# Optimization experiments

Hardware: AMD Instinct MI355X
Metric: run time of the kernel (lower is better)

## Reference

```python
import jax, jax.numpy as jnp
import numpy as np

E, I, D = 8, 2816, 1024   # num_experts, intermediate_size, dim
T, A = 1024, 2            # tokens, top-k experts per token


def setup_inputs() -> dict:
    key = jax.random.key(0)
    k1, k2, k3, k4, k5 = jax.random.split(key, 5)
    x = jax.random.normal(k1, (T, D), dtype=jnp.float32)
    expert_indices = jax.random.randint(k2, (T, A), 0, E, dtype=jnp.int64)
    scale = 0.02
    w1 = jax.random.normal(k3, (E, I, D), dtype=jnp.float32) * scale
    w2 = jax.random.normal(k4, (E, D, I), dtype=jnp.float32) * scale
    w3 = jax.random.normal(k5, (E, I, D), dtype=jnp.float32) * scale
    return {"x": x, "w1": w1, "w2": w2, "w3": w3, "expert_indices": expert_indices}


def reference(x, w1, w2, w3, expert_indices):
    # x: [T, D], expert_indices: [T, A]
    # Same math as torch: silu(x @ w1[e].T) * (x @ w3[e].T) @ w2[e].T per (t, a).
    # Compute all-expert projections once, then gather the selected expert rows
    # (avoids materializing the [T, A, I, D] per-token weight copies).
    idx = expert_indices.astype(jnp.int32)
    h1 = jnp.einsum('ti,eoi->teo', x, w1)              # [T, E, I]
    h3 = jnp.einsum('ti,eoi->teo', x, w3)              # [T, E, I]
    g1 = jnp.take_along_axis(h1, idx[:, :, None], axis=1)  # [T, A, I]
    g3 = jnp.take_along_axis(h3, idx[:, :, None], axis=1)  # [T, A, I]
    h = jax.nn.silu(g1) * g3                            # SwiGLU, [T, A, I]
    y_all = jnp.einsum('tao,eio->taei', h, w2)          # [T, A, E, D]
    out = jnp.take_along_axis(y_all, idx[:, :, None, None], axis=2)  # [T, A, 1, D]
    return out[:, :, 0, :]                              # [T, A, D]
```

## Files before the change

### kernel.cpp

```cpp
#include <hip/hip_runtime.h>
#include <hip/hip_bf16.h>

#define E_NUM 8
#define I_DIM 2816
#define D_DIM 1024
#define T_NUM 1024
#define A_TOP 2
#define NPAIR (T_NUM * A_TOP)
#define PADROWS 3072
#define MT_MAX (PADROWS / 128)

#define HB_OFF    16384ULL
#define HB_BYTES  ((unsigned long long)PADROWS * I_DIM * 2ULL)
#define XBF_OFF   (HB_OFF + HB_BYTES)
#define XBF_BYTES ((unsigned long long)T_NUM * D_DIM * 2ULL)
#define WS_NEED   (XBF_OFF + XBF_BYTES)

typedef __bf16 bf16x8 __attribute__((ext_vector_type(8)));
typedef float  f32x4  __attribute__((ext_vector_type(4)));

__device__ inline unsigned short f2bf(float f) {
  union { float f; unsigned u; } v; v.f = f;
  unsigned r = v.u + 0x7fffu + ((v.u >> 16) & 1u);
  return (unsigned short)(r >> 16);
}
__device__ inline uint4 pack8(float4 a, float4 b) {
  uint4 v;
  v.x = (unsigned)f2bf(a.x) | ((unsigned)f2bf(a.y) << 16);
  v.y = (unsigned)f2bf(a.z) | ((unsigned)f2bf(a.w) << 16);
  v.z = (unsigned)f2bf(b.x) | ((unsigned)f2bf(b.y) << 16);
  v.w = (unsigned)f2bf(b.z) | ((unsigned)f2bf(b.w) << 16);
  return v;
}
__device__ inline void gload_lds16(const unsigned short* g, unsigned short* l) {
  __builtin_amdgcn_global_load_lds((const __attribute__((address_space(1))) void*)g,
                                   (__attribute__((address_space(3))) void*)l, 16, 0, 0);
}

__global__ __launch_bounds__(256) void sort_pairs_kernel(
    const int* __restrict__ eidx, int* __restrict__ meta, int* __restrict__ pairs)
{
  __shared__ int cnt[E_NUM];
  __shared__ int pstart[E_NUM + 1];
  __shared__ int cur[E_NUM];
  int tid = threadIdx.x;
  if (tid < E_NUM) cnt[tid] = 0;
  __syncthreads();
  for (int p = tid; p < NPAIR; p += 256) atomicAdd(&cnt[eidx[p] & 7], 1);
  for (int i = tid; i < PADROWS; i += 256) pairs[i] = -1;
  __syncthreads();
  if (tid == 0) {
    int s = 0;
    for (int e = 0; e < E_NUM; ++e) {
      pstart[e] = s; cur[e] = s;
      s += ((cnt[e] + 127) / 128) * 128;
    }
    pstart[E_NUM] = s;
  }
  __syncthreads();
  for (int p = tid; p < NPAIR; p += 256) {
    int e = eidx[p] & 7;
    int pos = atomicAdd(&cur[e], 1);
    pairs[pos] = p;
  }
  __syncthreads();
  if (tid <= E_NUM) meta[tid] = pstart[tid];
}

__global__ __launch_bounds__(256) void convertx_kernel(
    const float* __restrict__ in, unsigned short* __restrict__ out)
{
  size_t i = (size_t)(blockIdx.x * 256 + threadIdx.x) * 8;
  const float4* p = (const float4*)(in + i);
  *(uint4*)(out + i) = pack8(p[0], p[1]);
}

__global__ __launch_bounds__(256, 2) void stage1_fused(
    const unsigned short* __restrict__ xbf, const float* __restrict__ w1,
    const float* __restrict__ w3, const int* __restrict__ meta,
    const int* __restrict__ pairs, unsigned short* __restrict__ hbuf)
{
  int mtile = blockIdx.y;
  int ptotal = meta[E_NUM];
  if (mtile * 128 >= ptotal) return;
  int e = 0;
  while (meta[e + 1] <= mtile * 128) ++e;
  int ntile = blockIdx.x;

  __shared__ alignas(16) unsigned short As[2][128 * 32];
  __shared__ alignas(16) unsigned short B1s[2][128 * 32];
  __shared__ alignas(16) unsigned short B3s[2][128 * 32];
  __shared__ int rowtok[128];

  int tid = threadIdx.x;
  for (int i = tid; i < 128; i += 256) {
    int p = pairs[mtile * 128 + i];
    rowtok[i] = (p >= 0) ? (p >> 1) : -1;
  }
  __syncthreads();

  int lane = tid & 63;
  int w = tid >> 6;
  int wm = w >> 1, wn = w & 1;
  int lrow = lane & 15, quad = lane >> 4;

  int lr4 = lane >> 2;
  int lc  = (lane & 3) * 8;
  int c0 = 2 * w;
  size_t aoff[2];
  const float* wb1[2];
  const float* wb3[2];
#pragma unroll
  for (int j = 0; j < 2; ++j) {
    int c = c0 + j;
    int r = c * 16 + lr4;
    int tok = rowtok[r]; if (tok < 0) tok = 0;
    aoff[j] = (size_t)tok * D_DIM + lc;
    int irow = ntile * 128 + r;
    wb1[j] = w1 + ((size_t)e * I_DIM + irow) * D_DIM + lc;
    wb3[j] = w3 + ((size_t)e * I_DIM + irow) * D_DIM + lc;
  }

  f32x4 acc1[4][4], acc3[4][4];
#pragma unroll
  for (int i = 0; i < 4; ++i)
#pragma unroll
    for (int j = 0; j < 4; ++j) {
      acc1[i][j] = (f32x4){0.f, 0.f, 0.f, 0.f};
      acc3[i][j] = (f32x4){0.f, 0.f, 0.f, 0.f};
    }

  float4 r1[2][2], r3[2][2];
#pragma unroll
  for (int j = 0; j < 2; ++j) {
    r1[j][0] = *(const float4*)(wb1[j]);
    r1[j][1] = *(const float4*)(wb1[j] + 4);
    r3[j][0] = *(const float4*)(wb3[j]);
    r3[j][1] = *(const float4*)(wb3[j] + 4);
    gload_lds16(xbf + aoff[j], &As[0][(c0 + j) * 512]);
  }
#pragma unroll
  for (int j = 0; j < 2; ++j) {
    *(uint4*)&B1s[0][(c0 + j) * 512 + lane * 8] = pack8(r1[j][0], r1[j][1]);
    *(uint4*)&B3s[0][(c0 + j) * 512 + lane * 8] = pack8(r3[j][0], r3[j][1]);
  }

  const int KT = D_DIM / 32;
  for (int k = 0; k < KT; ++k) {
    __syncthreads();
    int kk = k & 1;
    if (k + 1 < KT) {
      int kn = (k + 1) * 32;
#pragma unroll
      for (int j = 0; j < 2; ++j) {
        r1[j][0] = *(const float4*)(wb1[j] + kn);
        r1[j][1] = *(const float4*)(wb1[j] + kn + 4);
        r3[j][0] = *(const float4*)(wb3[j] + kn);
        r3[j][1] = *(const float4*)(wb3[j] + kn + 4);
        gload_lds16(xbf + aoff[j] + kn, &As[kk ^ 1][(c0 + j) * 512]);
      }
    }
    bf16x8 af[4];
#pragma unroll
    for (int mi = 0; mi < 4; ++mi)
      af[mi] = *(const bf16x8*)&As[kk][(wm * 64 + mi * 16 + lrow) * 32 + quad * 8];
#pragma unroll
    for (int ni = 0; ni < 4; ++ni) {
      bf16x8 b1 = *(const bf16x8*)&B1s[kk][(wn * 64 + ni * 16 + lrow) * 32 + quad * 8];
#pragma unroll
      for (int mi = 0; mi < 4; ++mi)
        acc1[mi][ni] = __builtin_amdgcn_mfma_f32_16x16x32_bf16(af[mi], b1, acc1[mi][ni], 0, 0, 0);
      bf16x8 b3 = *(const bf16x8*)&B3s[kk][(wn * 64 + ni * 16 + lrow) * 32 + quad * 8];
#pragma unroll
      for (int mi = 0; mi < 4; ++mi)
        acc3[mi][ni] = __builtin_amdgcn_mfma_f32_16x16x32_bf16(af[mi], b3, acc3[mi][ni], 0, 0, 0);
    }
    if (k + 1 < KT) {
#pragma unroll
      for (int j = 0; j < 2; ++j) {
        *(uint4*)&B1s[kk ^ 1][(c0 + j) * 512 + lane * 8] = pack8(r1[j][0], r1[j][1]);
        *(uint4*)&B3s[kk ^ 1][(c0 + j) * 512 + lane * 8] = pack8(r3[j][0], r3[j][1]);
      }
    }
  }

#pragma unroll
  for (int mi = 0; mi < 4; ++mi) {
#pragma unroll
    for (int r = 0; r < 4; ++r) {
      int lr = wm * 64 + mi * 16 + quad * 4 + r;
      if (rowtok[lr] >= 0) {
        size_t base = (size_t)(mtile * 128 + lr) * I_DIM + (size_t)ntile * 128 + wn * 64;
#pragma unroll
        for (int ni = 0; ni < 4; ++ni) {
          float v1 = acc1[mi][ni][r];
          float v3 = acc3[mi][ni][r];
          float hv = (v1 / (1.f + __expf(-v1))) * v3;
          hbuf[base + ni * 16 + lrow] = f2bf(hv);
        }
      }
    }
  }
}

__global__ __launch_bounds__(256, 4) void stage2_fused(
    const unsigned short* __restrict__ hbuf, const float* __restrict__ w2,
    const int* __restrict__ meta, const int* __restrict__ pairs,
    float* __restrict__ out)
{
  int mtile = blockIdx.y;
  int ptotal = meta[E_NUM];
  if (mtile * 128 >= ptotal) return;
  int e = 0;
  while (meta[e + 1] <= mtile * 128) ++e;
  int ntile = blockIdx.x;

  __shared__ alignas(16) unsigned short As[2][128 * 32];
  __shared__ alignas(16) unsigned short Bs[2][64 * 32];
  __shared__ int prow[128];

  int tid = threadIdx.x;
  for (int i = tid; i < 128; i += 256) {
    int grow = mtile * 128 + i;
    prow[i] = pairs[grow];
  }
  __syncthreads();

  int lane = tid & 63;
  int w = tid >> 6;
  int lrow = lane & 15, quad = lane >> 4;
  int lr4 = lane >> 2;
  int lc  = (lane & 3) * 8;
  int c0 = 2 * w;

  size_t aoff[2];
#pragma unroll
  for (int j = 0; j < 2; ++j)
    aoff[j] = (size_t)(mtile * 128 + (c0 + j) * 16 + lr4) * I_DIM + lc;
  const float* wb2 = w2 + ((size_t)e * D_DIM + ntile * 64 + w * 16 + lr4) * I_DIM + lc;

  f32x4 acc[2][4];
#pragma unroll
  for (int i = 0; i < 2; ++i)
#pragma unroll
    for (int j = 0; j < 4; ++j) acc[i][j] = (f32x4){0.f, 0.f, 0.f, 0.f};

  float4 rb[2];
  rb[0] = *(const float4*)(wb2);
  rb[1] = *(const float4*)(wb2 + 4);
#pragma unroll
  for (int j = 0; j < 2; ++j)
    gload_lds16(hbuf + aoff[j], &As[0][(c0 + j) * 512]);
  *(uint4*)&Bs[0][w * 512 + lane * 8] = pack8(rb[0], rb[1]);

  const int KT = I_DIM / 32;
  for (int k = 0; k < KT; ++k) {
    __syncthreads();
    int kk = k & 1;
    if (k + 1 < KT) {
      int kn = (k + 1) * 32;
      rb[0] = *(const float4*)(wb2 + kn);
      rb[1] = *(const float4*)(wb2 + kn + 4);
#pragma unroll
      for (int j = 0; j < 2; ++j)
        gload_lds16(hbuf + aoff[j] + kn, &As[kk ^ 1][(c0 + j) * 512]);
    }
    bf16x8 af0 = *(const bf16x8*)&As[kk][(w * 32 + lrow) * 32 + quad * 8];
    bf16x8 af1 = *(const bf16x8*)&As[kk][(w * 32 + 16 + lrow) * 32 + quad * 8];
#pragma unroll
    for (int ni = 0; ni < 4; ++ni) {
      bf16x8 bfr = *(const bf16x8*)&Bs[kk][(ni * 16 + lrow) * 32 + quad * 8];
      acc[0][ni] = __builtin_amdgcn_mfma_f32_16x16x32_bf16(af0, bfr, acc[0][ni], 0, 0, 0);
      acc[1][ni] = __builtin_amdgcn_mfma_f32_16x16x32_bf16(af1, bfr, acc[1][ni], 0, 0, 0);
    }
    if (k + 1 < KT)
      *(uint4*)&Bs[kk ^ 1][w * 512 + lane * 8] = pack8(rb[0], rb[1]);
  }

#pragma unroll
  for (int mi = 0; mi < 2; ++mi) {
#pragma unroll
    for (int r = 0; r < 4; ++r) {
      int lr = w * 32 + mi * 16 + quad * 4 + r;
      int p = prow[lr];
      if (p >= 0) {
        float* obase = out + (size_t)p * D_DIM + (size_t)ntile * 64;
#pragma unroll
        for (int ni = 0; ni < 4; ++ni)
          obase[ni * 16 + lrow] = acc[mi][ni][r];
      }
    }
  }
}

extern "C" void kernel_launch(void* const* d_in, const int* in_sizes, int n_in,
                              void* d_out, int out_size, void* d_ws, size_t ws_size,
                              hipStream_t stream) {
  const float* x  = (const float*)d_in[0];
  const float* w1 = (const float*)d_in[1];
  const float* w2 = (const float*)d_in[2];
  const float* w3 = (const float*)d_in[3];
  const int* eidx = (const int*)d_in[4];
  float* out = (float*)d_out;

  int* meta  = (int*)d_ws;
  int* pairs = (int*)((char*)d_ws + 64);
  unsigned short* hbuf = (unsigned short*)((char*)d_ws + HB_OFF);
  unsigned short* xbf  = (unsigned short*)((char*)d_ws + XBF_OFF);

  sort_pairs_kernel<<<1, 256, 0, stream>>>(eidx, meta, pairs);
  convertx_kernel<<<(T_NUM * D_DIM) / 8 / 256, 256, 0, stream>>>(x, xbf);

  dim3 g1(I_DIM / 128, MT_MAX);
  stage1_fused<<<g1, 256, 0, stream>>>(xbf, w1, w3, meta, pairs, hbuf);
  dim3 g2(D_DIM / 64, MT_MAX);
  stage2_fused<<<g2, 256, 0, stream>>>(hbuf, w2, meta, pairs, out);
}
```

Before: 384.8 us.

## Narrow stage1 tiles and split-K stage2 with atomic accumulation

Stage1 output tiles shrink from 128 to 64 intermediate columns, which doubles the grid and raises the occupancy hint to 3. Stage2 switches to 128x128 tiles with a 4-way split over the intermediate dimension. Partial sums are combined with float atomicAdd into an output that is zeroed by a new memset. The aim is more parallel blocks for the weight-streaming GEMMs. The cost is atomic traffic and a non-deterministic summation order in stage2, and stage1 now reloads the A tile for twice as many blocks.

```diff
diff --git a/kernel.cpp b/kernel.cpp
--- a/kernel.cpp
+++ b/kernel.cpp
@@ -9,12 +9,13 @@
 #define NPAIR (T_NUM * A_TOP)
 #define PADROWS 3072
 #define MT_MAX (PADROWS / 128)
+#define KSPLIT 4
+#define KCHUNK (I_DIM / KSPLIT)
+#define KT2 (KCHUNK / 32)
 
 #define HB_OFF    16384ULL
 #define HB_BYTES  ((unsigned long long)PADROWS * I_DIM * 2ULL)
 #define XBF_OFF   (HB_OFF + HB_BYTES)
-#define XBF_BYTES ((unsigned long long)T_NUM * D_DIM * 2ULL)
-#define WS_NEED   (XBF_OFF + XBF_BYTES)
 
 typedef __bf16 bf16x8 __attribute__((ext_vector_type(8)));
 typedef float  f32x4  __attribute__((ext_vector_type(4)));
@@ -75,21 +76,20 @@
   *(uint4*)(out + i) = pack8(p[0], p[1]);
 }
 
-__global__ __launch_bounds__(256, 2) void stage1_fused(
+__global__ __launch_bounds__(256, 3) void stage1_v4(
     const unsigned short* __restrict__ xbf, const float* __restrict__ w1,
     const float* __restrict__ w3, const int* __restrict__ meta,
     const int* __restrict__ pairs, unsigned short* __restrict__ hbuf)
 {
   int mtile = blockIdx.y;
-  int ptotal = meta[E_NUM];
-  if (mtile * 128 >= ptotal) return;
+  if (mtile * 128 >= meta[E_NUM]) return;
   int e = 0;
   while (meta[e + 1] <= mtile * 128) ++e;
   int ntile = blockIdx.x;
 
   __shared__ alignas(16) unsigned short As[2][128 * 32];
-  __shared__ alignas(16) unsigned short B1s[2][128 * 32];
-  __shared__ alignas(16) unsigned short B3s[2][128 * 32];
+  __shared__ alignas(16) unsigned short B1s[2][64 * 32];
+  __shared__ alignas(16) unsigned short B3s[2][64 * 32];
   __shared__ int rowtok[128];
 
   int tid = threadIdx.x;
@@ -99,51 +99,36 @@
   }
   __syncthreads();
 
-  int lane = tid & 63;
-  int w = tid >> 6;
-  int wm = w >> 1, wn = w & 1;
-  int lrow = lane & 15, quad = lane >> 4;
-
-  int lr4 = lane >> 2;
-  int lc  = (lane & 3) * 8;
-  int c0 = 2 * w;
-  size_t aoff[2];
-  const float* wb1[2];
-  const float* wb3[2];
+  int lane = tid & 63, w = tid >> 6;
+  int wm = w >> 1, wn = w & 1, lrow = lane & 15, quad = lane >> 4;
+
+  size_t axoff[2];
 #pragma unroll
   for (int j = 0; j < 2; ++j) {
-    int c = c0 + j;
-    int r = c * 16 + lr4;
+    int r = 32 * w + 16 * j + (lane >> 2);
     int tok = rowtok[r]; if (tok < 0) tok = 0;
-    aoff[j] = (size_t)tok * D_DIM + lc;
-    int irow = ntile * 128 + r;
-    wb1[j] = w1 + ((size_t)e * I_DIM + irow) * D_DIM + lc;
-    wb3[j] = w3 + ((size_t)e * I_DIM + irow) * D_DIM + lc;
-  }
-
-  f32x4 acc1[4][4], acc3[4][4];
+    axoff[j] = (size_t)tok * D_DIM + (lane & 3) * 8;
+  }
+  const float* pw1 = w1 + ((size_t)e * I_DIM + ntile * 64 + (tid >> 2)) * D_DIM + (tid & 3) * 8;
+  const float* pw3 = w3 + ((size_t)e * I_DIM + ntile * 64 + (tid >> 2)) * D_DIM + (tid & 3) * 8;
+  int bws = (tid >> 2) * 32 + (tid & 3) * 8;
+
+  f32x4 acc1[4][2], acc3[4][2];
 #pragma unroll
   for (int i = 0; i < 4; ++i)
 #pragma unroll
-    for (int j = 0; j < 4; ++j) {
+    for (int j = 0; j < 2; ++j) {
       acc1[i][j] = (f32x4){0.f, 0.f, 0.f, 0.f};
       acc3[i][j] = (f32x4){0.f, 0.f, 0.f, 0.f};
     }
 
-  float4 r1[2][2], r3[2][2];
-#pragma unroll
-  for (int j = 0; j < 2; ++j) {
-    r1[j][0] = *(const float4*)(wb1[j]);
-    r1[j][1] = *(const float4*)(wb1[j] + 4);
-    r3[j][0] = *(const float4*)(wb3[j]);
-    r3[j][1] = *(const float4*)(wb3[j] + 4);
-    gload_lds16(xbf + aoff[j], &As[0][(c0 + j) * 512]);
-  }
-#pragma unroll
-  for (int j = 0; j < 2; ++j) {
-    *(uint4*)&B1s[0][(c0 + j) * 512 + lane * 8] = pack8(r1[j][0], r1[j][1]);
-    *(uint4*)&B3s[0][(c0 + j) * 512 + lane * 8] = pack8(r3[j][0], r3[j][1]);
-  }
+  float4 r1[2], r3[2];
+  r1[0] = *(const float4*)(pw1);     r1[1] = *(const float4*)(pw1 + 4);
+  r3[0] = *(const float4*)(pw3);     r3[1] = *(const float4*)(pw3 + 4);
+  gload_lds16(xbf + axoff[0], &As[0][(32 * w) * 32]);
+  gload_lds16(xbf + axoff[1], &As[0][(32 * w + 16) * 32]);
+  *(uint4*)&B1s[0][bws] = pack8(r1[0], r1[1]);
+  *(uint4*)&B3s[0][bws] = pack8(r3[0], r3[1]);
 
   const int KT = D_DIM / 32;
   for (int k = 0; k < KT; ++k) {
@@ -151,36 +136,29 @@
     int kk = k & 1;
     if (k + 1 < KT) {
       int kn = (k + 1) * 32;
-#pragma unroll
-      for (int j = 0; j < 2; ++j) {
-        r1[j][0] = *(const float4*)(wb1[j] + kn);
-        r1[j][1] = *(const float4*)(wb1[j] + kn + 4);
-        r3[j][0] = *(const float4*)(wb3[j] + kn);
-        r3[j][1] = *(const float4*)(wb3[j] + kn + 4);
-        gload_lds16(xbf + aoff[j] + kn, &As[kk ^ 1][(c0 + j) * 512]);
-      }
+      r1[0] = *(const float4*)(pw1 + kn); r1[1] = *(const float4*)(pw1 + kn + 4);
+      r3[0] = *(const float4*)(pw3 + kn); r3[1] = *(const float4*)(pw3 + kn + 4);
+      gload_lds16(xbf + axoff[0] + kn, &As[kk ^ 1][(32 * w) * 32]);
+      gload_lds16(xbf + axoff[1] + kn, &As[kk ^ 1][(32 * w + 16) * 32]);
     }
     bf16x8 af[4];
 #pragma unroll
     for (int mi = 0; mi < 4; ++mi)
       af[mi] = *(const bf16x8*)&As[kk][(wm * 64 + mi * 16 + lrow) * 32 + quad * 8];
 #pragma unroll
-    for (int ni = 0; ni < 4; ++ni) {
-      bf16x8 b1 = *(const bf16x8*)&B1s[kk][(wn * 64 + ni * 16 + lrow) * 32 + quad * 8];
+    for (int ni = 0; ni < 2; ++ni) {
+      bf16x8 b1 = *(const bf16x8*)&B1s[kk][(wn * 32 + ni * 16 + lrow) * 32 + quad * 8];
 #pragma unroll
       for (int mi = 0; mi < 4; ++mi)
         acc1[mi][ni] = __builtin_amdgcn_mfma_f32_16x16x32_bf16(af[mi], b1, acc1[mi][ni], 0, 0, 0);
-      bf16x8 b3 = *(const bf16x8*)&B3s[kk][(wn * 64 + ni * 16 + lrow) * 32 + quad * 8];
+      bf16x8 b3 = *(const bf16x8*)&B3s[kk][(wn * 32 + ni * 16 + lrow) * 32 + quad * 8];
 #pragma unroll
       for (int mi = 0; mi < 4; ++mi)
         acc3[mi][ni] = __builtin_amdgcn_mfma_f32_16x16x32_bf16(af[mi], b3, acc3[mi][ni], 0, 0, 0);
     }
     if (k + 1 < KT) {
-#pragma unroll
-      for (int j = 0; j < 2; ++j) {
-        *(uint4*)&B1s[kk ^ 1][(c0 + j) * 512 + lane * 8] = pack8(r1[j][0], r1[j][1]);
-        *(uint4*)&B3s[kk ^ 1][(c0 + j) * 512 + lane * 8] = pack8(r3[j][0], r3[j][1]);
-      }
+      *(uint4*)&B1s[kk ^ 1][bws] = pack8(r1[0], r1[1]);
+      *(uint4*)&B3s[kk ^ 1][bws] = pack8(r3[0], r3[1]);
     }
   }
 
@@ -190,9 +168,9 @@
     for (int r = 0; r < 4; ++r) {
       int lr = wm * 64 + mi * 16 + quad * 4 + r;
       if (rowtok[lr] >= 0) {
-        size_t base = (size_t)(mtile * 128 + lr) * I_DIM + (size_t)ntile * 128 + wn * 64;
-#pragma unroll
-        for (int ni = 0; ni < 4; ++ni) {
+        size_t base = (size_t)(mtile * 128 + lr) * I_DIM + (size_t)ntile * 64 + wn * 32;
+#pragma unroll
+        for (int ni = 0; ni < 2; ++ni) {
           float v1 = acc1[mi][ni][r];
           float v3 = acc3[mi][ni][r];
           float hv = (v1 / (1.f + __expf(-v1))) * v3;
@@ -203,91 +181,102 @@
   }
 }
 
-__global__ __launch_bounds__(256, 4) void stage2_fused(
+__global__ __launch_bounds__(256, 3) void stage2_v4(
     const unsigned short* __restrict__ hbuf, const float* __restrict__ w2,
     const int* __restrict__ meta, const int* __restrict__ pairs,
     float* __restrict__ out)
 {
   int mtile = blockIdx.y;
-  int ptotal = meta[E_NUM];
-  if (mtile * 128 >= ptotal) return;
+  if (mtile * 128 >= meta[E_NUM]) return;
   int e = 0;
   while (meta[e + 1] <= mtile * 128) ++e;
   int ntile = blockIdx.x;
+  int kbase = blockIdx.z * KCHUNK;
 
   __shared__ alignas(16) unsigned short As[2][128 * 32];
-  __shared__ alignas(16) unsigned short Bs[2][64 * 32];
+  __shared__ alignas(16) unsigned short Bs[2][128 * 32];
   __shared__ int prow[128];
 
   int tid = threadIdx.x;
-  for (int i = tid; i < 128; i += 256) {
-    int grow = mtile * 128 + i;
-    prow[i] = pairs[grow];
-  }
-  __syncthreads();
-
-  int lane = tid & 63;
-  int w = tid >> 6;
-  int lrow = lane & 15, quad = lane >> 4;
-  int lr4 = lane >> 2;
-  int lc  = (lane & 3) * 8;
-  int c0 = 2 * w;
-
-  size_t aoff[2];
+  for (int i = tid; i < 128; i += 256) prow[i] = pairs[mtile * 128 + i];
+  __syncthreads();
+
+  int lane = tid & 63, w = tid >> 6;
+  int wm = w >> 1, wn = w & 1, lrow = lane & 15, quad = lane >> 4;
+
+  size_t axoff[2];
+#pragma unroll
+  for (int j = 0; j < 2; ++j) {
+    int r = 32 * w + 16 * j + (lane >> 2);
+    axoff[j] = (size_t)(mtile * 128 + r) * I_DIM + kbase + (lane & 3) * 8;
+  }
+  const float* pw2[2];
+  int bws[2];
+#pragma unroll
+  for (int j = 0; j < 2; ++j) {
+    int row = j * 64 + (tid >> 2);
+    pw2[j] = w2 + ((size_t)e * D_DIM + ntile * 128 + row) * I_DIM + kbase + (tid & 3) * 8;
+    bws[j] = row * 32 + (tid & 3) * 8;
+  }
+
+  f32x4 acc[4][4];
+#pragma unroll
+  for (int i = 0; i < 4; ++i)
+#pragma unroll
+    for (int j = 0; j < 4; ++j) acc[i][j] = (f32x4){0.f, 0.f, 0.f, 0.f};
+
+  float4 rb[2][2];
+#pragma unroll
+  for (int j = 0; j < 2; ++j) {
+    rb[j][0] = *(const float4*)(pw2[j]);
+    rb[j][1] = *(const float4*)(pw2[j] + 4);
+    gload_lds16(hbuf + axoff[j], &As[0][(32 * w + 16 * j) * 32]);
+  }
 #pragma unroll
   for (int j = 0; j < 2; ++j)
-    aoff[j] = (size_t)(mtile * 128 + (c0 + j) * 16 + lr4) * I_DIM + lc;
-  const float* wb2 = w2 + ((size_t)e * D_DIM + ntile * 64 + w * 16 + lr4) * I_DIM + lc;
-
-  f32x4 acc[2][4];
-#pragma unroll
-  for (int i = 0; i < 2; ++i)
-#pragma unroll
-    for (int j = 0; j < 4; ++j) acc[i][j] = (f32x4){0.f, 0.f, 0.f, 0.f};
-
-  float4 rb[2];
-  rb[0] = *(const float4*)(wb2);
-  rb[1] = *(const float4*)(wb2 + 4);
-#pragma unroll
-  for (int j = 0; j < 2; ++j)
-    gload_lds16(hbuf + aoff[j], &As[0][(c0 + j) * 512]);
-  *(uint4*)&Bs[0][w * 512 + lane * 8] = pack8(rb[0], rb[1]);
-
-  const int KT = I_DIM / 32;
-  for (int k = 0; k < KT; ++k) {
+    *(uint4*)&Bs[0][bws[j]] = pack8(rb[j][0], rb[j][1]);
+
+  for (int k = 0; k < KT2; ++k) {
     __syncthreads();
     int kk = k & 1;
-    if (k + 1 < KT) {
+    if (k + 1 < KT2) {
       int kn = (k + 1) * 32;
-      rb[0] = *(const float4*)(wb2 + kn);
-      rb[1] = *(const float4*)(wb2 + kn + 4);
+#pragma unroll
+      for (int j = 0; j < 2; ++j) {
+        rb[j][0] = *(const float4*)(pw2[j] + kn);
+        rb[j][1] = *(const float4*)(pw2[j] + kn + 4);
+        gload_lds16(hbuf + axoff[j] + kn, &As[kk ^ 1][(32 * w + 16 * j) * 32]);
+      }
+    }
+    bf16x8 af[4];
+#pragma unroll
+    for (int mi = 0; mi < 4; ++mi)
+      af[mi] = *(const bf16x8*)&As[kk][(wm * 64 + mi * 16 + lrow) * 32 + quad * 8];
+#pragma unroll
+    for (int ni = 0; ni < 4; ++ni) {
+      bf16x8 bfr = *(const bf16x8*)&Bs[kk][(wn * 64 + ni * 16 + lrow) * 32 + quad * 8];
+#pragma unroll
+      for (int mi = 0; mi < 4; ++mi)
+        acc[mi][ni] = __builtin_amdgcn_mfma_f32_16x16x32_bf16(af[mi], bfr, acc[mi][ni], 0, 0, 0);
+    }
+    if (k + 1 < KT2) {
 #pragma unroll
       for (int j = 0; j < 2; ++j)
-        gload_lds16(hbuf + aoff[j] + kn, &As[kk ^ 1][(c0 + j) * 512]);
-    }
-    bf16x8 af0 = *(const bf16x8*)&As[kk][(w * 32 + lrow) * 32 + quad * 8];
-    bf16x8 af1 = *(const bf16x8*)&As[kk][(w * 32 + 16 + lrow) * 32 + quad * 8];
-#pragma unroll
-    for (int ni = 0; ni < 4; ++ni) {
-      bf16x8 bfr = *(const bf16x8*)&Bs[kk][(ni * 16 + lrow) * 32 + quad * 8];
-      acc[0][ni] = __builtin_amdgcn_mfma_f32_16x16x32_bf16(af0, bfr, acc[0][ni], 0, 0, 0);
-      acc[1][ni] = __builtin_amdgcn_mfma_f32_16x16x32_bf16(af1, bfr, acc[1][ni], 0, 0, 0);
-    }
-    if (k + 1 < KT)
-      *(uint4*)&Bs[kk ^ 1][w * 512 + lane * 8] = pack8(rb[0], rb[1]);
-  }
-
-#pragma unroll
-  for (int mi = 0; mi < 2; ++mi) {
+        *(uint4*)&Bs[kk ^ 1][bws[j]] = pack8(rb[j][0], rb[j][1]);
+    }
+  }
+
+#pragma unroll
+  for (int mi = 0; mi < 4; ++mi) {
 #pragma unroll
     for (int r = 0; r < 4; ++r) {
-      int lr = w * 32 + mi * 16 + quad * 4 + r;
+      int lr = wm * 64 + mi * 16 + quad * 4 + r;
       int p = prow[lr];
       if (p >= 0) {
-        float* obase = out + (size_t)p * D_DIM + (size_t)ntile * 64;
+        float* obase = out + (size_t)p * D_DIM + (size_t)ntile * 128 + wn * 64;
 #pragma unroll
         for (int ni = 0; ni < 4; ++ni)
-          obase[ni * 16 + lrow] = acc[mi][ni][r];
+          atomicAdd(obase + ni * 16 + lrow, acc[mi][ni][r]);
       }
     }
   }
@@ -310,9 +299,10 @@
 
   sort_pairs_kernel<<<1, 256, 0, stream>>>(eidx, meta, pairs);
   convertx_kernel<<<(T_NUM * D_DIM) / 8 / 256, 256, 0, stream>>>(x, xbf);
-
-  dim3 g1(I_DIM / 128, MT_MAX);
-  stage1_fused<<<g1, 256, 0, stream>>>(xbf, w1, w3, meta, pairs, hbuf);
-  dim3 g2(D_DIM / 64, MT_MAX);
-  stage2_fused<<<g2, 256, 0, stream>>>(hbuf, w2, meta, pairs, out);
-}
+  hipMemsetAsync(out, 0, (size_t)out_size * sizeof(float), stream);
+
+  dim3 g1(I_DIM / 64, MT_MAX);
+  stage1_v4<<<g1, 256, 0, stream>>>(xbf, w1, w3, meta, pairs, hbuf);
+  dim3 g2(D_DIM / 128, MT_MAX, KSPLIT);
+  stage2_v4<<<g2, 256, 0, stream>>>(hbuf, w2, meta, pairs, out);
+}
```

Measured after the change: 348.2 us. 1.11x faster.
